# Performance work log

Hardware: AMD Instinct MI355X
Metric: run time of the kernel (lower is better)

Reference implementation:

```python
import jax, jax.numpy as jnp
import numpy as np

H = 32          # query heads
KV = 8          # kv heads
DH = 64         # head dim
WINDOW = 1024   # sliding window
BASE = 10000.0  # rope base


def _rope(x, pos):
    """Interleaved RoPE as in RotaryEmbedding.apply. x: (B,H,T,Dh), pos: (T,)."""
    inv = 1.0 / (BASE ** (jnp.arange(0, DH, 2, dtype=jnp.float32) / DH))  # (Dh/2,)
    freqs = pos.astype(jnp.float32)[:, None] * inv[None, :]               # (T, Dh/2)
    cos = jnp.cos(freqs)[None, None].astype(x.dtype)
    sin = jnp.sin(freqs)[None, None].astype(x.dtype)
    x1, x2 = x[..., ::2], x[..., 1::2]
    o1 = x1 * cos - x2 * sin
    o2 = x1 * sin + x2 * cos
    return jnp.stack([o1, o2], axis=-1).reshape(x.shape)


def setup_inputs() -> dict:
    key = jax.random.key(0)
    ks = jax.random.split(key, 5)
    B, T, D, Tc = 2, 4096, 2048, 4096
    x = jax.random.normal(ks[0], (B, T, D), jnp.float32)
    k_cache = jax.random.normal(ks[1], (B, KV, Tc, DH), jnp.float32)
    v_cache = jax.random.normal(ks[2], (B, KV, Tc, DH), jnp.float32)
    Wq = jax.random.normal(ks[3], (D, D), jnp.float32) * 0.02
    Wo = jax.random.normal(ks[4], (D, D), jnp.float32) * 0.02
    return {"x": x, "k_cache": k_cache, "v_cache": v_cache, "Wq": Wq, "Wo": Wo}


def reference(x, k_cache, v_cache, Wq, Wo):
    """AttnLayer.forward, role='follower', local=True, return_attn=False, eval mode."""
    B, T, D = x.shape
    rep = H // KV
    # q projection: nn.Linear(d, H*Dh, bias=False) -> x @ W.T
    q = (x @ Wq.T).reshape(B, T, H, DH).transpose(0, 2, 1, 3)  # (B,H,T,Dh)
    Tc = k_cache.shape[2]
    pos_q = jnp.arange(Tc - T, Tc)
    q = _rope(q, pos_q)
    # GQA: KV -> H head replication (repeat_interleave along head dim)
    k = jnp.repeat(k_cache, rep, axis=1)  # (B,H,Tc,Dh)
    v = jnp.repeat(v_cache, rep, axis=1)
    # sliding-window slice: keep last `window` keys
    w = min(WINDOW, Tc)
    k = k[:, :, Tc - w:, :]  # (B,H,Tk,Dh)
    v = v[:, :, Tc - w:, :]
    Tk = w
    scale = 1.0 / np.sqrt(DH).astype(np.float32)
    scores = jnp.einsum('bhtd,bhsd->bhts', q, k) * scale  # (B,H,T,Tk)
    # torch SDPA is_causal with L != S uses a TOP-LEFT aligned tril mask: j <= i
    causal = jnp.arange(Tk)[None, :] <= jnp.arange(T)[:, None]  # (T,Tk)
    scores = jnp.where(causal[None, None], scores, -jnp.inf)
    attn = jax.nn.softmax(scores, axis=-1)
    out = jnp.einsum('bhts,bhsd->bhtd', attn, v)
    out = out.transpose(0, 2, 1, 3).reshape(B, T, H * DH)
    return out @ Wo.T
```

## Files before the change

kernel.cpp:

```cpp
#include <hip/hip_runtime.h>
#include <math.h>

typedef __attribute__((ext_vector_type(8))) short short8;
typedef __attribute__((ext_vector_type(4))) float floatx4;
typedef __attribute__((ext_vector_type(4))) unsigned int uintx4;
typedef __attribute__((ext_vector_type(2))) unsigned int uintx2;

#define MFMA16(a, b, c) __builtin_amdgcn_mfma_f32_16x16x32_bf16((a), (b), (c), 0, 0, 0)

#define QSCALE 0.18033688011112042f

__device__ __forceinline__ unsigned short f2bf(float x) {
    unsigned int u = __float_as_uint(x);
    u += 0x7fffu + ((u >> 16) & 1u);
    return (unsigned short)(u >> 16);
}

__device__ __forceinline__ short8 lds8(const unsigned short* p) {
    return *reinterpret_cast<const short8*>(p);
}

__device__ __forceinline__ void g2l16(const unsigned short* g, unsigned short* l) {
    __builtin_amdgcn_global_load_lds(
        (const __attribute__((address_space(1))) unsigned int*)g,
        (__attribute__((address_space(3))) unsigned int*)l,
        16, 0, 0);
}

__device__ __forceinline__ unsigned int cvtpk(float a, float b) {
    unsigned int r;
    asm("v_cvt_pk_bf16_f32 %0, %1, %2" : "=v"(r) : "v"(a), "v"(b));
    return r;
}

__device__ __forceinline__ void pl32swap(unsigned int& a, unsigned int& b) {
    asm("v_permlane32_swap_b32 %0, %1" : "+v"(a), "+v"(b));
}

__device__ __forceinline__ void pl16swap(unsigned int& a, unsigned int& b) {
    asm("v_permlane16_swap_b32 %0, %1" : "+v"(a), "+v"(b));
}

__global__ void cvt_bf16(const float* __restrict__ src, unsigned short* __restrict__ dst, int n4) {
    int i = blockIdx.x * blockDim.x + threadIdx.x;
    if (i >= n4) return;
    float4 v = reinterpret_cast<const float4*>(src)[i];
    ushort4 o;
    o.x = f2bf(v.x); o.y = f2bf(v.y); o.z = f2bf(v.z); o.w = f2bf(v.w);
    reinterpret_cast<ushort4*>(dst)[i] = o;
}

__global__ void prep_k(const float* __restrict__ kc, unsigned short* __restrict__ Kw) {
    int i = blockIdx.x * blockDim.x + threadIdx.x;
    int d4  = (i & 15) * 4;
    int s   = (i >> 4) & 1023;
    int bkv = i >> 14;
    size_t src = ((size_t)bkv * 4096 + 3072 + s) * 64 + d4;
    float4 kv = *reinterpret_cast<const float4*>(kc + src);
    ushort4 ko;
    ko.x = f2bf(kv.x); ko.y = f2bf(kv.y); ko.z = f2bf(kv.z); ko.w = f2bf(kv.w);
    *reinterpret_cast<ushort4*>(Kw + ((size_t)bkv * 1024 + s) * 64 + d4) = ko;
}

__global__ void prep_v(const float* __restrict__ vc, unsigned short* __restrict__ Vt) {
    __shared__ unsigned short tl[64][72];
    const int bkv = blockIdx.x >> 4;
    const int s0  = (blockIdx.x & 15) * 64;
    const int t   = threadIdx.x;
    const int sl  = t >> 2;
    const int dq  = (t & 3) * 16;
    const float* src = vc + ((size_t)bkv * 4096 + 3072 + s0 + sl) * 64 + dq;
    float4 v0 = reinterpret_cast<const float4*>(src)[0];
    float4 v1 = reinterpret_cast<const float4*>(src)[1];
    float4 v2 = reinterpret_cast<const float4*>(src)[2];
    float4 v3 = reinterpret_cast<const float4*>(src)[3];
    tl[dq +  0][sl] = f2bf(v0.x); tl[dq +  1][sl] = f2bf(v0.y);
    tl[dq +  2][sl] = f2bf(v0.z); tl[dq +  3][sl] = f2bf(v0.w);
    tl[dq +  4][sl] = f2bf(v1.x); tl[dq +  5][sl] = f2bf(v1.y);
    tl[dq +  6][sl] = f2bf(v1.z); tl[dq +  7][sl] = f2bf(v1.w);
    tl[dq +  8][sl] = f2bf(v2.x); tl[dq +  9][sl] = f2bf(v2.y);
    tl[dq + 10][sl] = f2bf(v2.z); tl[dq + 11][sl] = f2bf(v2.w);
    tl[dq + 12][sl] = f2bf(v3.x); tl[dq + 13][sl] = f2bf(v3.y);
    tl[dq + 14][sl] = f2bf(v3.z); tl[dq + 15][sl] = f2bf(v3.w);
    __syncthreads();
    const int dl = t >> 2;
    const int sc = (t & 3) * 16;
    unsigned short* dst = Vt + ((size_t)bkv * 64 + dl) * 1024 + s0 + sc;
    short8 x0 = *reinterpret_cast<const short8*>(&tl[dl][sc]);
    short8 x1 = *reinterpret_cast<const short8*>(&tl[dl][sc + 8]);
    *reinterpret_cast<short8*>(dst)     = x0;
    *reinterpret_cast<short8*>(dst + 8) = x1;
}

template <int EPI>
__global__ __launch_bounds__(512, 2)
void gemm256(const unsigned short* __restrict__ A,
             const unsigned short* __restrict__ Bt,
             float* __restrict__ Cf,
             unsigned short* __restrict__ Cb) {
    constexpr int K  = 2048;
    constexpr int NT = 64;
    __shared__ unsigned short sm[32768];

    const int tid  = threadIdx.x;
    const int lane = tid & 63;
    const int l15  = lane & 15;
    const int quad = lane >> 4;
    const int wid  = tid >> 6;
    const int wr   = wid >> 2;
    const int wc   = wid & 3;

    const int bn = blockIdx.x & 7;
    const int bm = blockIdx.x >> 3;

    const unsigned short* gA0 = A  + (size_t)(bm * 256 + 2 * wid * 16 + l15) * K + quad * 8;
    const unsigned short* gA1 = gA0 + (size_t)16 * K;
    const unsigned short* gB0 = Bt + (size_t)(bn * 256 + 2 * wid * 16 + l15) * K + quad * 8;
    const unsigned short* gB1 = gB0 + (size_t)16 * K;

    auto STAGE = [&](int t) {
        unsigned short* dst = sm + (t & 1) * 16384 + 2 * wid * 512;
        const int off = t * 32;
        g2l16(gA0 + off, dst);
        g2l16(gA1 + off, dst + 512);
        g2l16(gB0 + off, dst + 8192);
        g2l16(gB1 + off, dst + 8704);
    };

    floatx4 acc[8][4];
#pragma unroll
    for (int i = 0; i < 8; ++i)
#pragma unroll
        for (int j = 0; j < 4; ++j) acc[i][j] = floatx4{0, 0, 0, 0};

    STAGE(0);
    STAGE(1);
    asm volatile("s_waitcnt vmcnt(4)" ::: "memory");
    __builtin_amdgcn_s_barrier();
    asm volatile("" ::: "memory");

    for (int t = 0; t < NT; ++t) {
        const unsigned short* cb = sm + (t & 1) * 16384;

        short8 bf[4], af[8];
#pragma unroll
        for (int j = 0; j < 4; ++j)
            bf[j] = lds8(cb + 8192 + (wc * 4 + j) * 512 + lane * 8);
#pragma unroll
        for (int i = 0; i < 8; ++i)
            af[i] = lds8(cb + (wr * 8 + i) * 512 + lane * 8);

        asm volatile("s_waitcnt lgkmcnt(0)" ::: "memory");
        __builtin_amdgcn_s_barrier();
        asm volatile("" ::: "memory");

        if (t + 2 < NT) STAGE(t + 2);

        __builtin_amdgcn_s_setprio(1);
#pragma unroll
        for (int i = 0; i < 8; ++i)
#pragma unroll
            for (int j = 0; j < 4; ++j)
                acc[i][j] = MFMA16(af[i], bf[j], acc[i][j]);
        __builtin_amdgcn_s_setprio(0);

        if (t + 2 < NT) asm volatile("s_waitcnt vmcnt(4)" ::: "memory");
        else            asm volatile("s_waitcnt vmcnt(0)" ::: "memory");
        __builtin_amdgcn_s_barrier();
        asm volatile("" ::: "memory");
    }

    float2* tabf = reinterpret_cast<float2*>(sm);
    if (EPI == 0) {
        const int t0 = (bm & 15) * 256;
        for (int e = tid; e < 8192; e += 512) {
            int tl = e >> 5, d2 = e & 31;
            float f = (float)(t0 + tl) * exp2f(-(float)d2 * 0.41524101186092f);
            float sn, cs; __sincosf(f, &sn, &cs);
            tabf[tl * 32 + d2] = make_float2(cs, sn);
        }
        __syncthreads();
    }

#pragma unroll
    for (int i = 0; i < 8; ++i)
#pragma unroll
        for (int j = 0; j < 4; ++j)
#pragma unroll
            for (int r = 0; r < 4; ++r) {
                int row = bm * 256 + wr * 128 + i * 16 + quad * 4 + r;
                int col = bn * 256 + wc * 64 + j * 16 + l15;
                float v = acc[i][j][r];
                if (EPI == 0) {
                    float p = __shfl_xor(v, 1);
                    int t_ = row & 4095, b_ = row >> 12;
                    int hh = col >> 6, d = col & 63;
                    int tl = wr * 128 + i * 16 + quad * 4 + r;
                    float2 cspair = tabf[tl * 32 + (d >> 1)];
                    float o = (d & 1) ? (p * cspair.y + v * cspair.x)
                                      : (v * cspair.x - p * cspair.y);
                    o *= QSCALE;
                    float po = __shfl_xor(o, 1);
                    if (!(lane & 1)) {
                        unsigned int pk = (unsigned int)f2bf(o) |
                                          ((unsigned int)f2bf(po) << 16);
                        *reinterpret_cast<unsigned int*>(
                            Cb + ((size_t)((b_ * 32 + hh) * 4096 + t_)) * 64 + d) = pk;
                    }
                } else {
                    Cf[(size_t)row * 2048 + col] = v;
                }
            }
}

__global__ __launch_bounds__(512, 8)
void attn(const unsigned short* __restrict__ Q,
          const unsigned short* __restrict__ Kw,
          const unsigned short* __restrict__ Vt,
          unsigned short* __restrict__ O) {
    const int blk  = blockIdx.x;
    const int qblk = blk & 31;
    const int bh   = blk >> 5;
    const int h    = bh & 31;
    const int b    = bh >> 5;
    const int kvh  = h >> 2;

    const int tid  = threadIdx.x;
    const int lane = tid & 63;
    const int l15  = lane & 15;
    const int quad = lane >> 4;
    const int wid  = tid >> 6;
    const int qt0  = qblk * 128 + wid * 16;

    const unsigned short* Qp = Q  + ((size_t)bh * 4096 + qt0) * 64;
    const unsigned short* Kp = Kw + (size_t)(b * 8 + kvh) * 1024 * 64;
    const unsigned short* Vp = Vt + (size_t)(b * 8 + kvh) * 64 * 1024;

    __shared__ unsigned short Ks[2][4096];
    __shared__ unsigned short Vs[2][4096];

    short8 qa0 = lds8(&Qp[l15 * 64 + quad * 8]);
    short8 qa1 = lds8(&Qp[l15 * 64 + 32 + quad * 8]);

    const unsigned short* gK = Kp + (size_t)((wid >> 1) * 16 + l15) * 64
                                  + (wid & 1) * 32 + quad * 8;
    const unsigned short* gV = Vp + (size_t)((wid >> 1) * 16 + l15) * 1024
                                  + (wid & 1) * 32 + quad * 8;
    unsigned short* sK0 = &Ks[0][wid * 512];
    unsigned short* sK1 = &Ks[1][wid * 512];
    unsigned short* sV0 = &Vs[0][wid * 512];
    unsigned short* sV1 = &Vs[1][wid * 512];

    const int ntiles = (qblk < 7 ? 2 * qblk + 2 : 16);
    const int nkW    = (qt0 + 16 < 1024) ? qt0 + 16 : 1024;
    const int ntW    = (nkW + 63) >> 6;
    const bool diagW = (qt0 < 1024);

    g2l16(gK, sK0);
    g2l16(gV, sV0);

    floatx4 o0 = {0,0,0,0}, o1 = {0,0,0,0}, o2 = {0,0,0,0}, o3 = {0,0,0,0};
    float Lq = 0.f;
    float m = -INFINITY;

    for (int it = 0; it < ntiles; ++it) {
        __syncthreads();
        const int cur = it & 1;
        if (it + 1 < ntiles) {
            g2l16(gK + (it + 1) * 4096, cur ? sK0 : sK1);
            g2l16(gV + (it + 1) * 64,   cur ? sV0 : sV1);
        }
        if (it >= ntW) continue;
        const int s0 = it << 6;
        const unsigned short* Kc = Ks[cur];
        const unsigned short* Vc = Vs[cur];

        floatx4 sS[4];
#pragma unroll
        for (int c = 0; c < 4; ++c) {
            floatx4 z = {0, 0, 0, 0};
            z = MFMA16(lds8(Kc + c * 1024 + lane * 8), qa0, z);
            z = MFMA16(lds8(Kc + c * 1024 + 512 + lane * 8), qa1, z);
            sS[c] = z;
        }

        const bool last = (it == ntW - 1);
        bool skipHi = false;
        if (last && diagW) {
#pragma unroll
            for (int c = 0; c < 4; ++c)
#pragma unroll
                for (int r = 0; r < 4; ++r)
                    if (s0 + c * 16 + quad * 4 + r > qt0 + l15) sS[c][r] = -INFINITY;
            skipHi = (nkW - s0 <= 32);
        }

        float t0 = fmaxf(fmaxf(sS[0][0], sS[0][1]), fmaxf(sS[0][2], sS[0][3]));
        float t1 = fmaxf(fmaxf(sS[1][0], sS[1][1]), fmaxf(sS[1][2], sS[1][3]));
        float t2 = fmaxf(fmaxf(sS[2][0], sS[2][1]), fmaxf(sS[2][2], sS[2][3]));
        float t3 = fmaxf(fmaxf(sS[3][0], sS[3][1]), fmaxf(sS[3][2], sS[3][3]));
        float mx = fmaxf(fmaxf(t0, t1), fmaxf(t2, t3));
        mx = fmaxf(mx, __shfl_xor(mx, 16));
        mx = fmaxf(mx, __shfl_xor(mx, 32));

        if (!__all(mx <= m + 8.0f)) {
            const float mn = fmaxf(m, mx);
            const float alpha = exp2f(m - mn);
            m = mn;
            o0 *= alpha; o1 *= alpha; o2 *= alpha; o3 *= alpha;
            Lq *= alpha;
        }

        float p[4][4];
#pragma unroll
        for (int c = 0; c < 4; ++c)
#pragma unroll
            for (int r = 0; r < 4; ++r) p[c][r] = exp2f(sS[c][r] - m);
        Lq += ((p[0][0] + p[0][1] + p[0][2] + p[0][3]) + (p[1][0] + p[1][1] + p[1][2] + p[1][3]))
            + ((p[2][0] + p[2][1] + p[2][2] + p[2][3]) + (p[3][0] + p[3][1] + p[3][2] + p[3][3]));

        unsigned int a0 = cvtpk(p[0][0], p[0][1]);
        unsigned int a1 = cvtpk(p[0][2], p[0][3]);
        unsigned int a2 = cvtpk(p[1][0], p[1][1]);
        unsigned int a3 = cvtpk(p[1][2], p[1][3]);
        pl32swap(a0, a2); pl32swap(a1, a3);
        pl16swap(a0, a2); pl16swap(a1, a3);
        uintx4 tlo = {a0, a1, a2, a3};
        short8 pa_lo = __builtin_bit_cast(short8, tlo);

        o0 = MFMA16(lds8(Vc + 0 * 512 + lane * 8), pa_lo, o0);
        o1 = MFMA16(lds8(Vc + 2 * 512 + lane * 8), pa_lo, o1);
        o2 = MFMA16(lds8(Vc + 4 * 512 + lane * 8), pa_lo, o2);
        o3 = MFMA16(lds8(Vc + 6 * 512 + lane * 8), pa_lo, o3);
        if (!skipHi) {
            unsigned int b0 = cvtpk(p[2][0], p[2][1]);
            unsigned int b1 = cvtpk(p[2][2], p[2][3]);
            unsigned int b2 = cvtpk(p[3][0], p[3][1]);
            unsigned int b3 = cvtpk(p[3][2], p[3][3]);
            pl32swap(b0, b2); pl32swap(b1, b3);
            pl16swap(b0, b2); pl16swap(b1, b3);
            uintx4 thi = {b0, b1, b2, b3};
            short8 pa_hi = __builtin_bit_cast(short8, thi);
            o0 = MFMA16(lds8(Vc + 1 * 512 + lane * 8), pa_hi, o0);
            o1 = MFMA16(lds8(Vc + 3 * 512 + lane * 8), pa_hi, o1);
            o2 = MFMA16(lds8(Vc + 5 * 512 + lane * 8), pa_hi, o2);
            o3 = MFMA16(lds8(Vc + 7 * 512 + lane * 8), pa_hi, o3);
        }
    }

    Lq += __shfl_xor(Lq, 16);
    Lq += __shfl_xor(Lq, 32);
    const float inv = 1.f / Lq;

    unsigned short* Op = O + (size_t)b * 4096 * 2048 + (size_t)(qt0 + l15) * 2048
                           + h * 64 + quad * 4;
    uintx2 w0, w1, w2, w3;
    w0.x = cvtpk(o0[0] * inv, o0[1] * inv); w0.y = cvtpk(o0[2] * inv, o0[3] * inv);
    w1.x = cvtpk(o1[0] * inv, o1[1] * inv); w1.y = cvtpk(o1[2] * inv, o1[3] * inv);
    w2.x = cvtpk(o2[0] * inv, o2[1] * inv); w2.y = cvtpk(o2[2] * inv, o2[3] * inv);
    w3.x = cvtpk(o3[0] * inv, o3[1] * inv); w3.y = cvtpk(o3[2] * inv, o3[3] * inv);
    *reinterpret_cast<uintx2*>(Op)      = w0;
    *reinterpret_cast<uintx2*>(Op + 16) = w1;
    *reinterpret_cast<uintx2*>(Op + 32) = w2;
    *reinterpret_cast<uintx2*>(Op + 48) = w3;
}

extern "C" void kernel_launch(void* const* d_in, const int* in_sizes, int n_in,
                              void* d_out, int out_size, void* d_ws, size_t ws_size,
                              hipStream_t stream) {
    const float* x  = (const float*)d_in[0];
    const float* kc = (const float*)d_in[1];
    const float* vc = (const float*)d_in[2];
    const float* Wq = (const float*)d_in[3];
    const float* Wo = (const float*)d_in[4];
    float* out = (float*)d_out;

    char* ws = (char*)d_ws;
    unsigned short* Xb  = (unsigned short*)(ws);
    unsigned short* Qb  = (unsigned short*)(ws + 33554432);
    unsigned short* Wqb = (unsigned short*)(ws + 67108864);
    unsigned short* Wob = (unsigned short*)(ws + 75497472);
    unsigned short* Kwb = (unsigned short*)(ws + 83886080);
    unsigned short* Vtb = (unsigned short*)(ws + 85983232);

    cvt_bf16<<<16384, 256, 0, stream>>>(x,  Xb,  4194304);
    cvt_bf16<<<4096,  256, 0, stream>>>(Wq, Wqb, 1048576);
    cvt_bf16<<<4096,  256, 0, stream>>>(Wo, Wob, 1048576);
    prep_k<<<1024, 256, 0, stream>>>(kc, Kwb);
    prep_v<<<256, 256, 0, stream>>>(vc, Vtb);

    gemm256<0><<<256, 512, 0, stream>>>(Xb, Wqb, nullptr, Qb);
    attn<<<2048, 512, 0, stream>>>(Qb, Kwb, Vtb, Xb);
    gemm256<1><<<256, 512, 0, stream>>>(Xb, Wob, out, nullptr);
}
```

Before: 444.1 us.

## Split GEMM k-step into two phases interleaving A/B staging with MFMA

Restructures the bf16 GEMM main loop so each k-tile runs as two half-phases. B fragments are loaded and MFMAs issued per half, while the next B tile and the tile-after-next A are staged between them. Loads are spread across the MFMA work instead of bunched at one point, which is meant to hide global-to-LDS latency better. The cost is more barriers per iteration and a different LDS layout, so synchronisation overhead may rise.

```diff
diff --git a/kernel.cpp b/kernel.cpp
--- a/kernel.cpp
+++ b/kernel.cpp
@@ -94,13 +94,13 @@
 
 template <int EPI>
 __global__ __launch_bounds__(512, 2)
-void gemm256(const unsigned short* __restrict__ A,
-             const unsigned short* __restrict__ Bt,
-             float* __restrict__ Cf,
-             unsigned short* __restrict__ Cb) {
-    constexpr int K  = 2048;
-    constexpr int NT = 64;
-    __shared__ unsigned short sm[32768];
+void gemm8p(const unsigned short* __restrict__ A,
+            const unsigned short* __restrict__ Bt,
+            float* __restrict__ Cf,
+            unsigned short* __restrict__ Cb) {
+    constexpr int K   = 2048;
+    constexpr int NKT = 64;
+    __shared__ __align__(16) unsigned short sm[32768];
 
     const int tid  = threadIdx.x;
     const int lane = tid & 63;
@@ -113,19 +113,13 @@
     const int bn = blockIdx.x & 7;
     const int bm = blockIdx.x >> 3;
 
-    const unsigned short* gA0 = A  + (size_t)(bm * 256 + 2 * wid * 16 + l15) * K + quad * 8;
-    const unsigned short* gA1 = gA0 + (size_t)16 * K;
-    const unsigned short* gB0 = Bt + (size_t)(bn * 256 + 2 * wid * 16 + l15) * K + quad * 8;
-    const unsigned short* gB1 = gB0 + (size_t)16 * K;
-
-    auto STAGE = [&](int t) {
-        unsigned short* dst = sm + (t & 1) * 16384 + 2 * wid * 512;
-        const int off = t * 32;
-        g2l16(gA0 + off, dst);
-        g2l16(gA1 + off, dst + 512);
-        g2l16(gB0 + off, dst + 8192);
-        g2l16(gB1 + off, dst + 8704);
-    };
+    const unsigned short* gA = A  + (size_t)(bm * 256 + wid * 16 + l15) * K + quad * 8;
+    const unsigned short* gB = Bt + (size_t)(bn * 256 + wid * 16 + l15) * K + quad * 8;
+
+#define STA(kt, h) g2l16(gA + (size_t)(h) * 128 * K + (kt) * 32, \
+                         sm + (((kt) & 1) * 2 + (h)) * 4096 + wid * 512)
+#define STB(kt, h) g2l16(gB + (size_t)(h) * 128 * K + (kt) * 32, \
+                         sm + 16384 + (((kt) & 1) * 2 + (h)) * 4096 + wid * 512)
 
     floatx4 acc[8][4];
 #pragma unroll
@@ -133,42 +127,53 @@
 #pragma unroll
         for (int j = 0; j < 4; ++j) acc[i][j] = floatx4{0, 0, 0, 0};
 
-    STAGE(0);
-    STAGE(1);
-    asm volatile("s_waitcnt vmcnt(4)" ::: "memory");
+    STA(0, 0); STA(0, 1); STB(0, 0); STB(0, 1); STA(1, 0); STA(1, 1);
+    asm volatile("s_waitcnt vmcnt(2)" ::: "memory");
     __builtin_amdgcn_s_barrier();
     asm volatile("" ::: "memory");
 
-    for (int t = 0; t < NT; ++t) {
-        const unsigned short* cb = sm + (t & 1) * 16384;
-
-        short8 bf[4], af[8];
-#pragma unroll
-        for (int j = 0; j < 4; ++j)
-            bf[j] = lds8(cb + 8192 + (wc * 4 + j) * 512 + lane * 8);
-#pragma unroll
-        for (int i = 0; i < 8; ++i)
-            af[i] = lds8(cb + (wr * 8 + i) * 512 + lane * 8);
-
-        asm volatile("s_waitcnt lgkmcnt(0)" ::: "memory");
+    for (int kt = 0; kt < NKT; ++kt) {
+        const int d = kt & 1;
+        const unsigned short* As = sm + (d * 2 + wr) * 4096;
+        const unsigned short* Bs = sm + 16384 + (d * 2 + (wc >> 1)) * 4096;
+
+        short8 af[8];
+#pragma unroll
+        for (int i = 0; i < 8; ++i) af[i] = lds8(As + i * 512 + lane * 8);
+        short8 bf0 = lds8(Bs + ((wc * 4 + 0) & 7) * 512 + lane * 8);
+        short8 bf1 = lds8(Bs + ((wc * 4 + 1) & 7) * 512 + lane * 8);
+        if (kt + 1 < NKT) { STB(kt + 1, 0); STB(kt + 1, 1); }
         __builtin_amdgcn_s_barrier();
         asm volatile("" ::: "memory");
-
-        if (t + 2 < NT) STAGE(t + 2);
-
         __builtin_amdgcn_s_setprio(1);
 #pragma unroll
-        for (int i = 0; i < 8; ++i)
-#pragma unroll
-            for (int j = 0; j < 4; ++j)
-                acc[i][j] = MFMA16(af[i], bf[j], acc[i][j]);
+        for (int i = 0; i < 8; ++i) {
+            acc[i][0] = MFMA16(af[i], bf0, acc[i][0]);
+            acc[i][1] = MFMA16(af[i], bf1, acc[i][1]);
+        }
         __builtin_amdgcn_s_setprio(0);
-
-        if (t + 2 < NT) asm volatile("s_waitcnt vmcnt(4)" ::: "memory");
-        else            asm volatile("s_waitcnt vmcnt(0)" ::: "memory");
+        __builtin_amdgcn_s_barrier();
+        asm volatile("" ::: "memory");
+
+        short8 bf2 = lds8(Bs + ((wc * 4 + 2) & 7) * 512 + lane * 8);
+        short8 bf3 = lds8(Bs + ((wc * 4 + 3) & 7) * 512 + lane * 8);
+        if (kt + 2 < NKT) { STA(kt + 2, 0); STA(kt + 2, 1); }
+        __builtin_amdgcn_s_barrier();
+        asm volatile("" ::: "memory");
+        __builtin_amdgcn_s_setprio(1);
+#pragma unroll
+        for (int i = 0; i < 8; ++i) {
+            acc[i][2] = MFMA16(af[i], bf2, acc[i][2]);
+            acc[i][3] = MFMA16(af[i], bf3, acc[i][3]);
+        }
+        __builtin_amdgcn_s_setprio(0);
+        if (kt + 2 < NKT) asm volatile("s_waitcnt vmcnt(2)" ::: "memory");
+        else              asm volatile("s_waitcnt vmcnt(0)" ::: "memory");
         __builtin_amdgcn_s_barrier();
         asm volatile("" ::: "memory");
     }
+#undef STA
+#undef STB
 
     float2* tabf = reinterpret_cast<float2*>(sm);
     if (EPI == 0) {
@@ -194,18 +199,18 @@
                 if (EPI == 0) {
                     float p = __shfl_xor(v, 1);
                     int t_ = row & 4095, b_ = row >> 12;
-                    int hh = col >> 6, d = col & 63;
+                    int hh = col >> 6, d_ = col & 63;
                     int tl = wr * 128 + i * 16 + quad * 4 + r;
-                    float2 cspair = tabf[tl * 32 + (d >> 1)];
-                    float o = (d & 1) ? (p * cspair.y + v * cspair.x)
-                                      : (v * cspair.x - p * cspair.y);
+                    float2 cspair = tabf[tl * 32 + (d_ >> 1)];
+                    float o = (d_ & 1) ? (p * cspair.y + v * cspair.x)
+                                       : (v * cspair.x - p * cspair.y);
                     o *= QSCALE;
                     float po = __shfl_xor(o, 1);
                     if (!(lane & 1)) {
                         unsigned int pk = (unsigned int)f2bf(o) |
                                           ((unsigned int)f2bf(po) << 16);
                         *reinterpret_cast<unsigned int*>(
-                            Cb + ((size_t)((b_ * 32 + hh) * 4096 + t_)) * 64 + d) = pk;
+                            Cb + ((size_t)((b_ * 32 + hh) * 4096 + t_)) * 64 + d_) = pk;
                     }
                 } else {
                     Cf[(size_t)row * 2048 + col] = v;
@@ -389,7 +394,7 @@
     prep_k<<<1024, 256, 0, stream>>>(kc, Kwb);
     prep_v<<<256, 256, 0, stream>>>(vc, Vtb);
 
-    gemm256<0><<<256, 512, 0, stream>>>(Xb, Wqb, nullptr, Qb);
+    gemm8p<0><<<256, 512, 0, stream>>>(Xb, Wqb, nullptr, Qb);
     attn<<<2048, 512, 0, stream>>>(Qb, Kwb, Vtb, Xb);
-    gemm256<1><<<256, 512, 0, stream>>>(Xb, Wob, out, nullptr);
-}
+    gemm8p<1><<<256, 512, 0, stream>>>(Xb, Wob, out, nullptr);
+}
```

Result: slower. 456.0 us (+2.7%).
